# Performance work log

Hardware: AMD Instinct MI355X
Metric: run time of the kernel (lower is better)

The kernel has to match this reference:

```python
import jax, jax.numpy as jnp
import numpy as np

B, S, D, H = 4, 2048, 1024, 16
DK = D // H


def setup_inputs() -> dict:
    key = jax.random.key(0)
    ks = jax.random.split(key, 5)
    scale = 1.0 / np.sqrt(D)
    return {
        "x": jax.random.normal(ks[0], (B, S, D), dtype=jnp.float32),
        "W_Q": jax.random.normal(ks[1], (D, D), dtype=jnp.float32) * scale,
        "W_K": jax.random.normal(ks[2], (D, D), dtype=jnp.float32) * scale,
        "W_V": jax.random.normal(ks[3], (D, D), dtype=jnp.float32) * scale,
        "W_O": jax.random.normal(ks[4], (D, D), dtype=jnp.float32) * scale,
    }


def reference(x, W_Q, W_K, W_V, W_O):
    b, s, d = x.shape
    # torch Linear convention: y = x @ W.T  (no bias in this assignment's Linear)
    q = (x @ W_Q.T).reshape(b, s, H, DK).transpose(0, 2, 1, 3)  # [b,h,s,dk]
    k = (x @ W_K.T).reshape(b, s, H, DK).transpose(0, 2, 1, 3)
    v = (x @ W_V.T).reshape(b, s, H, DK).transpose(0, 2, 1, 3)
    scores = jnp.einsum("bhqd,bhkd->bhqk", q, k) / jnp.sqrt(jnp.float32(DK))
    causal = jnp.tril(jnp.ones((s, s), dtype=bool))  # True where attention allowed
    scores = jnp.where(causal, scores, jnp.finfo(scores.dtype).min)
    attn = jax.nn.softmax(scores, axis=-1)
    out = jnp.einsum("bhqk,bhkd->bhqd", attn, v)
    out = out.transpose(0, 2, 1, 3).reshape(b, s, d)
    return out @ W_O.T
```

## Files before the change

### kernel.cpp

```cpp
#include <hip/hip_runtime.h>
#include <hip/hip_bf16.h>

#define BB 4
#define SS 2048
#define DD 1024
#define HH 16
#define DKK 64

typedef __attribute__((ext_vector_type(8))) short short8;
typedef __attribute__((ext_vector_type(4))) float f32x4;

typedef const __attribute__((address_space(1))) void gvoid;
typedef __attribute__((address_space(3))) void lvoid;

__device__ __forceinline__ unsigned short f2bf(float f) {
  unsigned int u = __builtin_bit_cast(unsigned int, f);
  u = (u + 0x7FFFu + ((u >> 16) & 1u)) >> 16;
  return (unsigned short)u;
}

__device__ __forceinline__ unsigned short f2bf_hw(float f) {
  return __builtin_bit_cast(unsigned short, __float2bfloat16(f));
}

__global__ __launch_bounds__(256) void convert_f32_bf16(
    const float* __restrict__ in, unsigned short* __restrict__ out, int n4) {
  int i = blockIdx.x * blockDim.x + threadIdx.x;
  if (i >= n4) return;
  float4 v = reinterpret_cast<const float4*>(in)[i];
  ushort4 o;
  o.x = f2bf(v.x); o.y = f2bf(v.y); o.z = f2bf(v.z); o.w = f2bf(v.w);
  reinterpret_cast<ushort4*>(out)[i] = o;
}

__global__ __launch_bounds__(256) void convert_w4(
    const float* __restrict__ a, const float* __restrict__ b,
    const float* __restrict__ c, const float* __restrict__ d,
    unsigned short* __restrict__ out, int n4) {
  int m = blockIdx.y;
  const float* src = (m == 0) ? a : (m == 1) ? b : (m == 2) ? c : d;
  int i = blockIdx.x * blockDim.x + threadIdx.x;
  if (i >= n4) return;
  float4 v = reinterpret_cast<const float4*>(src)[i];
  ushort4 o;
  o.x = f2bf(v.x); o.y = f2bf(v.y); o.z = f2bf(v.z); o.w = f2bf(v.w);
  reinterpret_cast<ushort4*>(out)[(size_t)m * n4 + i] = o;
}

__global__ __launch_bounds__(256) void gemm_qkv(
    const unsigned short* __restrict__ A,
    const unsigned short* __restrict__ Bm,
    unsigned short* __restrict__ Qo,
    unsigned short* __restrict__ Ko,
    unsigned short* __restrict__ Vo)
{
  __shared__ unsigned short As[128 * 32];
  __shared__ unsigned short Bs[128 * 32];
  const int K = DD;
  int bid = blockIdx.x;
  int m0 = (bid / 24) << 7;
  int n0 = (bid % 24) << 7;
  int t = threadIdx.x;
  int lane = t & 63, w = t >> 6;
  int l16 = lane & 15, lhi = lane >> 4;
  int wm = (w >> 1) * 64, wn = (w & 1) * 64;

  f32x4 acc[4][4];
#pragma unroll
  for (int i = 0; i < 4; ++i)
#pragma unroll
    for (int j = 0; j < 4; ++j) acc[i][j] = (f32x4){0.f, 0.f, 0.f, 0.f};

  for (int kt = 0; kt < K; kt += 32) {
    __syncthreads();
#pragma unroll
    for (int is = 0; is < 2; ++is) {
      int c = is * 256 + t;
      __builtin_amdgcn_global_load_lds(
          (gvoid*)(A + (size_t)(m0 + (c >> 2)) * K + kt + ((c & 3) << 3)),
          (lvoid*)(As + (size_t)(is * 256 + w * 64) * 8), 16, 0, 0);
      __builtin_amdgcn_global_load_lds(
          (gvoid*)(Bm + (size_t)(n0 + (c >> 2)) * K + kt + ((c & 3) << 3)),
          (lvoid*)(Bs + (size_t)(is * 256 + w * 64) * 8), 16, 0, 0);
    }
    __syncthreads();
    short8 af[4], bfr[4];
#pragma unroll
    for (int mf = 0; mf < 4; ++mf)
      af[mf] = *(const short8*)(As + (wm + mf * 16 + l16) * 32 + lhi * 8);
#pragma unroll
    for (int nf = 0; nf < 4; ++nf)
      bfr[nf] = *(const short8*)(Bs + (wn + nf * 16 + l16) * 32 + lhi * 8);
#pragma unroll
    for (int mf = 0; mf < 4; ++mf)
#pragma unroll
      for (int nf = 0; nf < 4; ++nf)
        acc[mf][nf] = __builtin_amdgcn_mfma_f32_16x16x32_bf16(
            af[mf], bfr[nf], acc[mf][nf], 0, 0, 0);
  }

  int mat = n0 >> 10;
  int nb = n0 & 1023;
  const float qscale = 0.18033688011112042f;
#pragma unroll
  for (int mf = 0; mf < 4; ++mf)
#pragma unroll
    for (int nf = 0; nf < 4; ++nf)
#pragma unroll
      for (int i = 0; i < 4; ++i) {
        int r = m0 + wm + mf * 16 + lhi * 4 + i;
        int c1 = nb + wn + nf * 16 + l16;
        int b = r >> 11, s = r & 2047;
        int h = c1 >> 6, dk = c1 & 63;
        if (mat == 0)
          Qo[((size_t)((b * HH + h) * SS + s) << 6) + dk] =
              f2bf(acc[mf][nf][i] * qscale);
        else if (mat == 1)
          Ko[((size_t)((b * HH + h) * SS + s) << 6) + dk] = f2bf(acc[mf][nf][i]);
        else
          Vo[(size_t)((b * HH + h) * DKK + dk) * SS + s] = f2bf(acc[mf][nf][i]);
      }
}

__global__ __launch_bounds__(256) void gemm_wo(
    const unsigned short* __restrict__ A,
    const unsigned short* __restrict__ Bm,
    float* __restrict__ C, int N, int K)
{
  __shared__ unsigned short As[128 * 32];
  __shared__ unsigned short Bs[128 * 32];
  int bid = blockIdx.x;
  int ntn = N >> 7;
  int m0 = (bid / ntn) << 7;
  int n0 = (bid % ntn) << 7;
  int t = threadIdx.x;
  int lane = t & 63, w = t >> 6;
  int l16 = lane & 15, lhi = lane >> 4;
  int wm = (w >> 1) * 64, wn = (w & 1) * 64;

  f32x4 acc[4][4];
#pragma unroll
  for (int i = 0; i < 4; ++i)
#pragma unroll
    for (int j = 0; j < 4; ++j) acc[i][j] = (f32x4){0.f, 0.f, 0.f, 0.f};

  for (int kt = 0; kt < K; kt += 32) {
    __syncthreads();
#pragma unroll
    for (int is = 0; is < 2; ++is) {
      int c = is * 256 + t;
      __builtin_amdgcn_global_load_lds(
          (gvoid*)(A + (size_t)(m0 + (c >> 2)) * K + kt + ((c & 3) << 3)),
          (lvoid*)(As + (size_t)(is * 256 + w * 64) * 8), 16, 0, 0);
      __builtin_amdgcn_global_load_lds(
          (gvoid*)(Bm + (size_t)(n0 + (c >> 2)) * K + kt + ((c & 3) << 3)),
          (lvoid*)(Bs + (size_t)(is * 256 + w * 64) * 8), 16, 0, 0);
    }
    __syncthreads();
    short8 af[4], bfr[4];
#pragma unroll
    for (int mf = 0; mf < 4; ++mf)
      af[mf] = *(const short8*)(As + (wm + mf * 16 + l16) * 32 + lhi * 8);
#pragma unroll
    for (int nf = 0; nf < 4; ++nf)
      bfr[nf] = *(const short8*)(Bs + (wn + nf * 16 + l16) * 32 + lhi * 8);
#pragma unroll
    for (int mf = 0; mf < 4; ++mf)
#pragma unroll
      for (int nf = 0; nf < 4; ++nf)
        acc[mf][nf] = __builtin_amdgcn_mfma_f32_16x16x32_bf16(
            af[mf], bfr[nf], acc[mf][nf], 0, 0, 0);
  }

#pragma unroll
  for (int mf = 0; mf < 4; ++mf)
#pragma unroll
    for (int nf = 0; nf < 4; ++nf)
#pragma unroll
      for (int i = 0; i < 4; ++i) {
        int r = m0 + wm + mf * 16 + lhi * 4 + i;
        int cc = n0 + wn + nf * 16 + l16;
        C[(size_t)r * N + cc] = acc[mf][nf][i];
      }
}

__global__ __launch_bounds__(256, 2) void attn_kernel(
    const unsigned short* __restrict__ Qh,
    const unsigned short* __restrict__ Kh,
    const unsigned short* __restrict__ Vt,
    unsigned short* __restrict__ O)
{
  __shared__ unsigned short Plds[4][32 * 72];

  int bid = blockIdx.x;
  int bh = bid & 63;
  int qb = 15 - (bid >> 6);
  int q0 = qb << 7;
  int t = threadIdx.x, lane = t & 63, w = t >> 6;
  int l16 = lane & 15, lhi = lane >> 4;
  int wq0 = q0 + w * 32;

  const unsigned short* Qb = Qh + (size_t)bh * SS * DKK;
  const unsigned short* Kb = Kh + (size_t)bh * SS * DKK;
  const unsigned short* Vb = Vt + (size_t)bh * SS * DKK;

  short8 aq[2][2];
#pragma unroll
  for (int qf = 0; qf < 2; ++qf)
#pragma unroll
    for (int kc = 0; kc < 2; ++kc)
      aq[qf][kc] = *(const short8*)(Qb + (size_t)(wq0 + qf * 16 + l16) * DKK +
                                    kc * 32 + lhi * 8);

  f32x4 oacc[2][4], acc1[2];
#pragma unroll
  for (int qf = 0; qf < 2; ++qf) {
    acc1[qf] = (f32x4){0.f, 0.f, 0.f, 0.f};
#pragma unroll
    for (int d = 0; d < 4; ++d) oacc[qf][d] = (f32x4){0.f, 0.f, 0.f, 0.f};
  }

  short8 ones;
  {
    short ov = (l16 == 0) ? (short)0x3F80 : (short)0;
#pragma unroll
    for (int j = 0; j < 8; ++j) ones[j] = ov;
  }

  int nt = (wq0 >> 6) + 1;

  short8 bk[4][2], bv[4][2];
#pragma unroll
  for (int sf = 0; sf < 4; ++sf)
#pragma unroll
    for (int kc = 0; kc < 2; ++kc)
      bk[sf][kc] = *(const short8*)(Kb + (size_t)(sf * 16 + l16) * DKK +
                                    kc * 32 + lhi * 8);
#pragma unroll
  for (int d = 0; d < 4; ++d)
#pragma unroll
    for (int kc = 0; kc < 2; ++kc)
      bv[d][kc] = *(const short8*)(Vb + (size_t)(d * 16 + l16) * SS +
                                   kc * 32 + lhi * 8);

  for (int tt = 0; tt < nt; ++tt) {
    int kv0 = tt << 6;
    f32x4 sacc[2][4];
#pragma unroll
    for (int qf = 0; qf < 2; ++qf)
#pragma unroll
      for (int sf = 0; sf < 4; ++sf) {
        sacc[qf][sf] = (f32x4){0.f, 0.f, 0.f, 0.f};
        sacc[qf][sf] = __builtin_amdgcn_mfma_f32_16x16x32_bf16(
            aq[qf][0], bk[sf][0], sacc[qf][sf], 0, 0, 0);
        sacc[qf][sf] = __builtin_amdgcn_mfma_f32_16x16x32_bf16(
            aq[qf][1], bk[sf][1], sacc[qf][sf], 0, 0, 0);
      }
    if (tt + 1 < nt) {
      int nk = kv0 + 64;
#pragma unroll
      for (int sf = 0; sf < 4; ++sf)
#pragma unroll
        for (int kc = 0; kc < 2; ++kc)
          bk[sf][kc] = *(const short8*)(Kb + (size_t)(nk + sf * 16 + l16) * DKK +
                                        kc * 32 + lhi * 8);
    }
    bool lastT = (tt == nt - 1);
#pragma unroll
    for (int qf = 0; qf < 2; ++qf)
#pragma unroll
      for (int sf = 0; sf < 4; ++sf)
#pragma unroll
        for (int i = 0; i < 4; ++i) {
          float p = exp2f(sacc[qf][sf][i] - 16.0f);
          if (lastT) {
            int key = kv0 + sf * 16 + l16;
            int qr = wq0 + qf * 16 + lhi * 4 + i;
            if (key > qr) p = 0.f;
          }
          Plds[w][(qf * 16 + lhi * 4 + i) * 72 + sf * 16 + l16] = f2bf_hw(p);
        }
    short8 ap[2][2];
#pragma unroll
    for (int qf = 0; qf < 2; ++qf)
#pragma unroll
      for (int kc = 0; kc < 2; ++kc)
        ap[qf][kc] = *(const short8*)(&Plds[w][(qf * 16 + l16) * 72 + kc * 32 + lhi * 8]);
#pragma unroll
    for (int qf = 0; qf < 2; ++qf)
#pragma unroll
      for (int kc = 0; kc < 2; ++kc)
        acc1[qf] = __builtin_amdgcn_mfma_f32_16x16x32_bf16(
            ap[qf][kc], ones, acc1[qf], 0, 0, 0);
#pragma unroll
    for (int qf = 0; qf < 2; ++qf)
#pragma unroll
      for (int d = 0; d < 4; ++d)
#pragma unroll
        for (int kc = 0; kc < 2; ++kc)
          oacc[qf][d] = __builtin_amdgcn_mfma_f32_16x16x32_bf16(
              ap[qf][kc], bv[d][kc], oacc[qf][d], 0, 0, 0);
    if (tt + 1 < nt) {
      int nk = kv0 + 64;
#pragma unroll
      for (int d = 0; d < 4; ++d)
#pragma unroll
        for (int kc = 0; kc < 2; ++kc)
          bv[d][kc] = *(const short8*)(Vb + (size_t)(d * 16 + l16) * SS + nk +
                                       kc * 32 + lhi * 8);
    }
  }

  int b = bh >> 4, h = bh & 15;
#pragma unroll
  for (int qf = 0; qf < 2; ++qf)
#pragma unroll
    for (int i = 0; i < 4; ++i) {
      float l = __shfl(acc1[qf][i], lane & 48);
      float inv = 1.0f / l;
      int s = wq0 + qf * 16 + lhi * 4 + i;
#pragma unroll
      for (int d = 0; d < 4; ++d)
        O[(size_t)(b * SS + s) * DD + h * DKK + d * 16 + l16] =
            f2bf(oacc[qf][d][i] * inv);
    }
}

extern "C" void kernel_launch(void* const* d_in, const int* in_sizes, int n_in,
                              void* d_out, int out_size, void* d_ws, size_t ws_size,
                              hipStream_t stream) {
  const float* x  = (const float*)d_in[0];
  const float* WQ = (const float*)d_in[1];
  const float* WK = (const float*)d_in[2];
  const float* WV = (const float*)d_in[3];
  const float* WO = (const float*)d_in[4];
  float* out = (float*)d_out;

  const size_t NX = (size_t)BB * SS * DD;
  const size_t NW = (size_t)DD * DD;

  unsigned short* xb   = (unsigned short*)d_ws;
  unsigned short* wcat = xb + NX;
  unsigned short* wo   = wcat + 3 * NW;
  unsigned short* Qh   = wcat + 4 * NW;
  unsigned short* Kh   = Qh + NX;
  unsigned short* Vt   = Kh + NX;
  unsigned short* attn = Vt + NX;

  convert_f32_bf16<<<(int)(NX / 4 / 256), 256, 0, stream>>>(x, xb, (int)(NX / 4));
  convert_w4<<<dim3((unsigned)(NW / 4 / 256), 4), 256, 0, stream>>>(
      WQ, WK, WV, WO, wcat, (int)(NW / 4));

  gemm_qkv<<<64 * 24, 256, 0, stream>>>(xb, wcat, Qh, Kh, Vt);

  attn_kernel<<<BB * HH * (SS / 128), 256, 0, stream>>>(Qh, Kh, Vt, attn);

  gemm_wo<<<64 * 8, 256, 0, stream>>>(attn, wo, out, DD, DD);
}
```

Baseline: 356.4 us.

## Pair mirrored 16-row query strips per wave to balance causal attention work

Each wave now handles two 16-row query strips, one near the start and one near the end of the sequence (s and 127-s), instead of two adjacent 16-row strips. This gives every wave and block roughly equal causal key-loop length, removing load imbalance between early and late query blocks. K/V tiles loaded per iteration are shared by both strips while the short strip is active, but once it finishes the MFMA work per K/V load is halved. It also adds branches on the active flag inside the loop.

```diff
diff --git a/kernel.cpp b/kernel.cpp
--- a/kernel.cpp
+++ b/kernel.cpp
@@ -194,30 +194,34 @@
 
   int bid = blockIdx.x;
   int bh = bid & 63;
-  int qb = 15 - (bid >> 6);
-  int q0 = qb << 7;
+  int sg = bid >> 6;
   int t = threadIdx.x, lane = t & 63, w = t >> 6;
   int l16 = lane & 15, lhi = lane >> 4;
-  int wq0 = q0 + w * 32;
+  int s = sg * 4 + w;
+  int rowA = s << 4;
+  int rowB = (127 - s) << 4;
+  int ntA = (s >> 2) + 1;
+  int ntB = ((127 - s) >> 2) + 1;
 
   const unsigned short* Qb = Qh + (size_t)bh * SS * DKK;
   const unsigned short* Kb = Kh + (size_t)bh * SS * DKK;
   const unsigned short* Vb = Vt + (size_t)bh * SS * DKK;
-
-  short8 aq[2][2];
-#pragma unroll
-  for (int qf = 0; qf < 2; ++qf)
-#pragma unroll
-    for (int kc = 0; kc < 2; ++kc)
-      aq[qf][kc] = *(const short8*)(Qb + (size_t)(wq0 + qf * 16 + l16) * DKK +
-                                    kc * 32 + lhi * 8);
-
-  f32x4 oacc[2][4], acc1[2];
-#pragma unroll
-  for (int qf = 0; qf < 2; ++qf) {
-    acc1[qf] = (f32x4){0.f, 0.f, 0.f, 0.f};
-#pragma unroll
-    for (int d = 0; d < 4; ++d) oacc[qf][d] = (f32x4){0.f, 0.f, 0.f, 0.f};
+  int b = bh >> 4, h = bh & 15;
+
+  short8 aqA[2], aqB[2];
+#pragma unroll
+  for (int kc = 0; kc < 2; ++kc) {
+    aqA[kc] = *(const short8*)(Qb + (size_t)(rowA + l16) * DKK + kc * 32 + lhi * 8);
+    aqB[kc] = *(const short8*)(Qb + (size_t)(rowB + l16) * DKK + kc * 32 + lhi * 8);
+  }
+
+  f32x4 oaccA[4], oaccB[4], acc1A, acc1B;
+  acc1A = (f32x4){0.f, 0.f, 0.f, 0.f};
+  acc1B = (f32x4){0.f, 0.f, 0.f, 0.f};
+#pragma unroll
+  for (int d = 0; d < 4; ++d) {
+    oaccA[d] = (f32x4){0.f, 0.f, 0.f, 0.f};
+    oaccB[d] = (f32x4){0.f, 0.f, 0.f, 0.f};
   }
 
   short8 ones;
@@ -227,8 +231,6 @@
     for (int j = 0; j < 8; ++j) ones[j] = ov;
   }
 
-  int nt = (wq0 >> 6) + 1;
-
   short8 bk[4][2], bv[4][2];
 #pragma unroll
   for (int sf = 0; sf < 4; ++sf)
@@ -243,20 +245,29 @@
       bv[d][kc] = *(const short8*)(Vb + (size_t)(d * 16 + l16) * SS +
                                    kc * 32 + lhi * 8);
 
-  for (int tt = 0; tt < nt; ++tt) {
+  for (int tt = 0; tt < ntB; ++tt) {
     int kv0 = tt << 6;
-    f32x4 sacc[2][4];
-#pragma unroll
-    for (int qf = 0; qf < 2; ++qf)
+    bool actA = (tt < ntA);
+    f32x4 saccB[4], saccA[4];
+#pragma unroll
+    for (int sf = 0; sf < 4; ++sf) {
+      saccB[sf] = (f32x4){0.f, 0.f, 0.f, 0.f};
+      saccB[sf] = __builtin_amdgcn_mfma_f32_16x16x32_bf16(
+          aqB[0], bk[sf][0], saccB[sf], 0, 0, 0);
+      saccB[sf] = __builtin_amdgcn_mfma_f32_16x16x32_bf16(
+          aqB[1], bk[sf][1], saccB[sf], 0, 0, 0);
+    }
+    if (actA) {
 #pragma unroll
       for (int sf = 0; sf < 4; ++sf) {
-        sacc[qf][sf] = (f32x4){0.f, 0.f, 0.f, 0.f};
-        sacc[qf][sf] = __builtin_amdgcn_mfma_f32_16x16x32_bf16(
-            aq[qf][0], bk[sf][0], sacc[qf][sf], 0, 0, 0);
-        sacc[qf][sf] = __builtin_amdgcn_mfma_f32_16x16x32_bf16(
-            aq[qf][1], bk[sf][1], sacc[qf][sf], 0, 0, 0);
+        saccA[sf] = (f32x4){0.f, 0.f, 0.f, 0.f};
+        saccA[sf] = __builtin_amdgcn_mfma_f32_16x16x32_bf16(
+            aqA[0], bk[sf][0], saccA[sf], 0, 0, 0);
+        saccA[sf] = __builtin_amdgcn_mfma_f32_16x16x32_bf16(
+            aqA[1], bk[sf][1], saccA[sf], 0, 0, 0);
       }
-    if (tt + 1 < nt) {
+    }
+    if (tt + 1 < ntB) {
       int nk = kv0 + 64;
 #pragma unroll
       for (int sf = 0; sf < 4; ++sf)
@@ -265,42 +276,63 @@
           bk[sf][kc] = *(const short8*)(Kb + (size_t)(nk + sf * 16 + l16) * DKK +
                                         kc * 32 + lhi * 8);
     }
-    bool lastT = (tt == nt - 1);
-#pragma unroll
-    for (int qf = 0; qf < 2; ++qf)
+    bool maskB = (tt == ntB - 1);
+#pragma unroll
+    for (int sf = 0; sf < 4; ++sf)
+#pragma unroll
+      for (int i = 0; i < 4; ++i) {
+        float p = exp2f(saccB[sf][i] - 16.0f);
+        if (maskB) {
+          int key = kv0 + sf * 16 + l16;
+          int qr = rowB + lhi * 4 + i;
+          if (key > qr) p = 0.f;
+        }
+        Plds[w][(16 + lhi * 4 + i) * 72 + sf * 16 + l16] = f2bf_hw(p);
+      }
+    if (actA) {
+      bool maskA = (tt == ntA - 1);
 #pragma unroll
       for (int sf = 0; sf < 4; ++sf)
 #pragma unroll
         for (int i = 0; i < 4; ++i) {
-          float p = exp2f(sacc[qf][sf][i] - 16.0f);
-          if (lastT) {
+          float p = exp2f(saccA[sf][i] - 16.0f);
+          if (maskA) {
             int key = kv0 + sf * 16 + l16;
-            int qr = wq0 + qf * 16 + lhi * 4 + i;
+            int qr = rowA + lhi * 4 + i;
             if (key > qr) p = 0.f;
           }
-          Plds[w][(qf * 16 + lhi * 4 + i) * 72 + sf * 16 + l16] = f2bf_hw(p);
+          Plds[w][(lhi * 4 + i) * 72 + sf * 16 + l16] = f2bf_hw(p);
         }
-    short8 ap[2][2];
-#pragma unroll
-    for (int qf = 0; qf < 2; ++qf)
+    }
+    short8 apB[2];
+#pragma unroll
+    for (int kc = 0; kc < 2; ++kc)
+      apB[kc] = *(const short8*)(&Plds[w][(16 + l16) * 72 + kc * 32 + lhi * 8]);
+#pragma unroll
+    for (int kc = 0; kc < 2; ++kc)
+      acc1B = __builtin_amdgcn_mfma_f32_16x16x32_bf16(apB[kc], ones, acc1B, 0, 0, 0);
+#pragma unroll
+    for (int d = 0; d < 4; ++d)
 #pragma unroll
       for (int kc = 0; kc < 2; ++kc)
-        ap[qf][kc] = *(const short8*)(&Plds[w][(qf * 16 + l16) * 72 + kc * 32 + lhi * 8]);
-#pragma unroll
-    for (int qf = 0; qf < 2; ++qf)
+        oaccB[d] = __builtin_amdgcn_mfma_f32_16x16x32_bf16(
+            apB[kc], bv[d][kc], oaccB[d], 0, 0, 0);
+    if (actA) {
+      short8 apA[2];
 #pragma unroll
       for (int kc = 0; kc < 2; ++kc)
-        acc1[qf] = __builtin_amdgcn_mfma_f32_16x16x32_bf16(
-            ap[qf][kc], ones, acc1[qf], 0, 0, 0);
-#pragma unroll
-    for (int qf = 0; qf < 2; ++qf)
+        apA[kc] = *(const short8*)(&Plds[w][l16 * 72 + kc * 32 + lhi * 8]);
+#pragma unroll
+      for (int kc = 0; kc < 2; ++kc)
+        acc1A = __builtin_amdgcn_mfma_f32_16x16x32_bf16(apA[kc], ones, acc1A, 0, 0, 0);
 #pragma unroll
       for (int d = 0; d < 4; ++d)
 #pragma unroll
         for (int kc = 0; kc < 2; ++kc)
-          oacc[qf][d] = __builtin_amdgcn_mfma_f32_16x16x32_bf16(
-              ap[qf][kc], bv[d][kc], oacc[qf][d], 0, 0, 0);
-    if (tt + 1 < nt) {
+          oaccA[d] = __builtin_amdgcn_mfma_f32_16x16x32_bf16(
+              apA[kc], bv[d][kc], oaccA[d], 0, 0, 0);
+    }
+    if (tt + 1 < ntB) {
       int nk = kv0 + 64;
 #pragma unroll
       for (int d = 0; d < 4; ++d)
@@ -311,19 +343,21 @@
     }
   }
 
-  int b = bh >> 4, h = bh & 15;
-#pragma unroll
-  for (int qf = 0; qf < 2; ++qf)
-#pragma unroll
-    for (int i = 0; i < 4; ++i) {
-      float l = __shfl(acc1[qf][i], lane & 48);
-      float inv = 1.0f / l;
-      int s = wq0 + qf * 16 + lhi * 4 + i;
-#pragma unroll
-      for (int d = 0; d < 4; ++d)
-        O[(size_t)(b * SS + s) * DD + h * DKK + d * 16 + l16] =
-            f2bf(oacc[qf][d][i] * inv);
-    }
+#pragma unroll
+  for (int i = 0; i < 4; ++i) {
+    float lA = __shfl(acc1A[i], lane & 48);
+    float lB = __shfl(acc1B[i], lane & 48);
+    float invA = 1.0f / lA, invB = 1.0f / lB;
+    int sA = rowA + lhi * 4 + i;
+    int sB = rowB + lhi * 4 + i;
+#pragma unroll
+    for (int d = 0; d < 4; ++d) {
+      O[(size_t)(b * SS + sA) * DD + h * DKK + d * 16 + l16] =
+          f2bf(oaccA[d][i] * invA);
+      O[(size_t)(b * SS + sB) * DD + h * DKK + d * 16 + l16] =
+          f2bf(oaccB[d][i] * invB);
+    }
+  }
 }
 
 extern "C" void kernel_launch(void* const* d_in, const int* in_sizes, int n_in,
@@ -353,7 +387,7 @@
 
   gemm_qkv<<<64 * 24, 256, 0, stream>>>(xb, wcat, Qh, Kh, Vt);
 
-  attn_kernel<<<BB * HH * (SS / 128), 256, 0, stream>>>(Qh, Kh, Vt, attn);
+  attn_kernel<<<64 * 16, 256, 0, stream>>>(Qh, Kh, Vt, attn);
 
   gemm_wo<<<64 * 8, 256, 0, stream>>>(attn, wo, out, DD, DD);
 }
```

New measurement: 407.9 us. +14.5%, slower.
